# Kernel tuning notes

Measured on AMD Instinct MI355X. Metric: run time of the kernel, lower is better.

## Reference

```python
import jax, jax.numpy as jnp
import numpy as np

B, S, D = 2, 2048, 1024
H = 16
HD = D // H  # 64


def setup_inputs() -> dict:
    key = jax.random.key(0)
    k1, k2, k3, k4, k5, k6 = jax.random.split(key, 6)
    hidden_states = jax.random.normal(k1, (B, S, D), dtype=jnp.float32)
    attention_mask = jax.random.randint(k2, (B, S), 0, 2, dtype=jnp.int32)
    scale = 1.0 / np.sqrt(D)
    Wq = jax.random.normal(k3, (D, D), dtype=jnp.float32) * scale
    bq = jax.random.normal(k4, (D,), dtype=jnp.float32) * 0.02
    Wk = jax.random.normal(k5, (D, D), dtype=jnp.float32) * scale
    bk = jax.random.normal(k6, (D,), dtype=jnp.float32) * 0.02
    return {"hidden_states": hidden_states, "attention_mask": attention_mask,
            "Wq": Wq, "bq": bq, "Wk": Wk, "bk": bk}


def _split_heads(x):
    # [B, S, D] -> [B, H, S, HD]
    b, s, _ = x.shape
    return x.reshape(b, s, H, HD).transpose(0, 2, 1, 3)


def reference(hidden_states, attention_mask, Wq, bq, Wk, bk):
    dh = jnp.sqrt(jnp.float32(HD))
    q = _split_heads(hidden_states @ Wq + bq)            # [B,H,S,HD]
    k = _split_heads(hidden_states @ Wk + bk)            # [B,H,S,HD]
    v = q + k                                            # value = Q + K
    k_t = -jax.nn.log_sigmoid(-k)                        # negate the logsigmoid(-K) transform
    scores = jnp.einsum('bhqd,bhkd->bhqk', q, k_t) / dh  # [B,H,S,S]
    # mask applied on the QUERY axis (dim 2), broadcast over key axis (faithful to source)
    mask = (attention_mask[:, None, :, None] == 0)       # [B,1,S,1]
    scores = jnp.where(mask, jnp.float32(-10000.0), scores)
    probs = jax.nn.softmax(scores, axis=-1)              # dropout: eval mode (identity)
    ctx = jnp.einsum('bhqk,bhkd->bhqd', probs, v)        # [B,H,S,HD]
    ctx = ctx.transpose(0, 2, 1, 3).reshape(B, S, D)
    return ctx
```

## Files before the change

### kernel.cpp

```cpp
#include <hip/hip_runtime.h>
#include <hip/hip_bf16.h>

#define B_ 2
#define S_ 2048
#define D_ 1024
#define H_ 16
#define HD_ 64

typedef __attribute__((ext_vector_type(8))) short short8;
typedef __attribute__((ext_vector_type(4))) short short4v;
typedef __attribute__((ext_vector_type(4))) float float4v;

typedef const __attribute__((address_space(1))) void* gas_ptr;
typedef __attribute__((address_space(3))) void* las_ptr;

static __device__ inline void gl_lds16(const void* g, void* l) {
  __builtin_amdgcn_global_load_lds((gas_ptr)g, (las_ptr)l, 16, 0, 0);
}

static __device__ inline float b2f(__hip_bfloat16 h) { return __bfloat162float(h); }

static __device__ inline short f2bs(float x) {
  __hip_bfloat16 h = __float2bfloat16(x);
  union { __hip_bfloat16 h; short s; } u; u.h = h; return u.s;
}
static __device__ inline float bs2f(short s) {
  union { short s; __hip_bfloat16 h; } u; u.s = s; return __bfloat162float(u.h);
}
static __device__ inline short4v pk4(float a, float b, float c, float d) {
  union { __hip_bfloat162 h[2]; short4v s; } u;
  u.h[0] = __float22bfloat162_rn(float2{a, b});
  u.h[1] = __float22bfloat162_rn(float2{c, d});
  return u.s;
}

static __device__ inline float4v mfma32(short8 a, short8 b, float4v c) {
  return __builtin_amdgcn_mfma_f32_16x16x32_bf16(a, b, c, 0, 0, 0);
}
static __device__ inline float4v mfma16(short4v a, short4v b, float4v c) {
  return __builtin_amdgcn_mfma_f32_16x16x16bf16_1k(a, b, c, 0, 0, 0);
}

__global__ __launch_bounds__(256) void pre(
    const float* __restrict__ Wq, const float* __restrict__ Wk,
    __hip_bfloat16* __restrict__ Wqt, __hip_bfloat16* __restrict__ Wkt) {
  const float* W = blockIdx.z ? Wk : Wq;
  __hip_bfloat16* Wt = blockIdx.z ? Wkt : Wqt;
  __shared__ float t[64][65];
  const int n0 = blockIdx.x * 64, k0 = blockIdx.y * 64;
  const int c = threadIdx.x & 63, r0 = threadIdx.x >> 6;
  for (int i = 0; i < 16; ++i) {
    const int r = i * 4 + r0;
    t[c][r] = W[(size_t)(k0 + r) * D_ + n0 + c];
  }
  __syncthreads();
  for (int i = 0; i < 16; ++i) {
    const int rr = i * 4 + r0;
    Wt[(size_t)(n0 + rr) * D_ + k0 + c] = __float2bfloat16(t[rr][c]);
  }
}

__global__ __launch_bounds__(512, 2) void gemm_fused(
    const float* __restrict__ hs,
    const __hip_bfloat16* __restrict__ Wqt, const __hip_bfloat16* __restrict__ Wkt,
    const float* __restrict__ bq, const float* __restrict__ bk,
    __hip_bfloat16* __restrict__ q_out, __hip_bfloat16* __restrict__ kt_out,
    __hip_bfloat16* __restrict__ vT) {
  const int id = blockIdx.x;
  const int mt = (id & 7) * 4 + ((id >> 3) & 3);
  const int nt = id >> 5;
  const int n0 = nt * 128, m0 = mt * 128;
  __shared__ __hip_bfloat16 As[2][128 * 32];
  __shared__ __hip_bfloat16 Bq[2][128 * 32];
  __shared__ __hip_bfloat16 Bk[2][128 * 32];
  const int tid = threadIdx.x, wid = tid >> 6, lane = tid & 63;
  const int wm = (wid >> 1) * 32, wn = (wid & 1) * 64;
  const int l15 = lane & 15, l4 = lane >> 4;
  const float4v zz = {0.f, 0.f, 0.f, 0.f};
  float4v accq[2][4], acck[2][4];
  for (int i = 0; i < 2; ++i)
    for (int j = 0; j < 4; ++j) { accq[i][j] = zz; acck[i][j] = zz; }
  const int lrow = wid * 16 + (lane >> 2);
  const int lk8 = (lane & 3) * 8;
  {
    const float* pa = hs + (size_t)(m0 + lrow) * D_ + lk8;
    const float4v a0 = ((const float4v*)pa)[0], a1 = ((const float4v*)pa)[1];
    short8 s;
    for (int j = 0; j < 4; ++j) { s[j] = f2bs(a0[j]); s[4 + j] = f2bs(a1[j]); }
    *(short8*)(As[0] + wid * 512 + lane * 8) = s;
    gl_lds16(Wqt + (size_t)(n0 + lrow) * D_ + lk8, Bq[0] + wid * 512);
    gl_lds16(Wkt + (size_t)(n0 + lrow) * D_ + lk8, Bk[0] + wid * 512);
  }
  int p = 0;
  for (int kb = 0; kb < 32; ++kb) {
    __syncthreads();
    if (kb < 31) {
      const int kc = (kb + 1) * 32 + lk8;
      gl_lds16(Wqt + (size_t)(n0 + lrow) * D_ + kc, Bq[p ^ 1] + wid * 512);
      gl_lds16(Wkt + (size_t)(n0 + lrow) * D_ + kc, Bk[p ^ 1] + wid * 512);
      const float* pa = hs + (size_t)(m0 + lrow) * D_ + kc;
      const float4v a0 = ((const float4v*)pa)[0], a1 = ((const float4v*)pa)[1];
      short8 s;
      for (int j = 0; j < 4; ++j) { s[j] = f2bs(a0[j]); s[4 + j] = f2bs(a1[j]); }
      *(short8*)(As[p ^ 1] + wid * 512 + lane * 8) = s;
    }
    short8 af[2], bfq[4], bfk[4];
    const int fo = l4 * 8;
    for (int rt = 0; rt < 2; ++rt)
      af[rt] = *(const short8*)(As[p] + (wm + rt * 16 + l15) * 32 + fo);
    for (int ct = 0; ct < 4; ++ct) {
      bfq[ct] = *(const short8*)(Bq[p] + (wn + ct * 16 + l15) * 32 + fo);
      bfk[ct] = *(const short8*)(Bk[p] + (wn + ct * 16 + l15) * 32 + fo);
    }
    for (int rt = 0; rt < 2; ++rt)
      for (int ct = 0; ct < 4; ++ct) {
        accq[rt][ct] = mfma32(af[rt], bfq[ct], accq[rt][ct]);
        acck[rt][ct] = mfma32(af[rt], bfk[ct], acck[rt][ct]);
      }
    p ^= 1;
  }
  float bvq[4], bvk[4];
  for (int ct = 0; ct < 4; ++ct) {
    bvq[ct] = bq[n0 + wn + ct * 16 + l15];
    bvk[ct] = bk[n0 + wn + ct * 16 + l15];
  }
  for (int rt = 0; rt < 2; ++rt)
    for (int ct = 0; ct < 4; ++ct) {
      const int col = n0 + wn + ct * 16 + l15;
      const int h = col >> 6, d = col & 63;
      const int rowb = m0 + wm + rt * 16 + l4 * 4;
      short4v vv;
      for (int r = 0; r < 4; ++r) {
        const int row = rowb + r;
        const float qv = accq[rt][ct][r] + bvq[ct];
        const float kv = acck[rt][ct][r] + bvk[ct];
        const float sp = fmaxf(kv, 0.f) + __logf(1.f + __expf(-fabsf(kv)));
        q_out[(size_t)row * D_ + col] = __float2bfloat16(qv);
        kt_out[(size_t)row * D_ + col] = __float2bfloat16(sp);
        vv[r] = f2bs(qv + kv);
      }
      const int b = rowb >> 11, s = rowb & 2047;
      const int sw = (s & ~63) | (((s >> 4) & 3) << 2) | (((s >> 2) & 3) << 4);
      *(short4v*)(vT + ((size_t)(b * H_ + h) * HD_ + d) * S_ + sw) = vv;
    }
}

__global__ __launch_bounds__(256, 2) void attn(
    const __hip_bfloat16* __restrict__ qb, const __hip_bfloat16* __restrict__ ktb,
    const __hip_bfloat16* __restrict__ vT, const int* __restrict__ mask,
    float* __restrict__ out) {
  __shared__ short smem[32768];
  const int id = blockIdx.x;
  const int xcd = id & 7;
  const int rest = id >> 3;
  const int q0 = (rest & 15) * 128;
  const int hb = (rest >> 4) * 8 + xcd;
  const int h = hb >> 1, b = hb & 1;
  const int tid = threadIdx.x, wid = tid >> 6, lane = tid & 63;
  const int l15 = lane & 15, l4 = lane >> 4;
  const __hip_bfloat16* qh = qb + (size_t)b * S_ * D_ + h * HD_;
  const __hip_bfloat16* kh = ktb + (size_t)b * S_ * D_ + h * HD_;
  const __hip_bfloat16* vh = vT + (size_t)(b * H_ + h) * HD_ * S_;
  const int srow = tid >> 2;
  const int b0 = tid & 3;
  const int sh = srow & 7;
  const int w0 = srow * 64 + ((b0 ^ sh) * 8);
  const int w1 = srow * 64 + (((b0 + 4) ^ sh) * 8);

  const int qlA = wid * 32 + l15, qlB = qlA + 16;
  const int qrA = q0 + qlA, qrB = q0 + qlB;
  const float SC = 0.125f * 1.44269504f;
  const float mqA = (mask[b * S_ + qrA] != 0) ? SC : 0.f;
  const float mqB = (mask[b * S_ + qrB] != 0) ? SC : 0.f;
  const short8 rA0 = *(const short8*)(qh + (size_t)qrA * D_ + l4 * 8);
  const short8 rA1 = *(const short8*)(qh + (size_t)qrA * D_ + 32 + l4 * 8);
  const short8 rB0 = *(const short8*)(qh + (size_t)qrB * D_ + l4 * 8);
  const short8 rB1 = *(const short8*)(qh + (size_t)qrB * D_ + 32 + l4 * 8);
  short8 bqA0, bqA1, bqB0, bqB1;
  for (int j = 0; j < 8; ++j) {
    bqA0[j] = f2bs(bs2f(rA0[j]) * mqA);
    bqA1[j] = f2bs(bs2f(rA1[j]) * mqA);
    bqB0[j] = f2bs(bs2f(rB0[j]) * mqB);
    bqB1[j] = f2bs(bs2f(rB1[j]) * mqB);
  }

  const int lsh = l15 & 7;
  const int ak0off = l15 * 64 + ((l4 ^ lsh) * 8);
  const int ak1off = l15 * 64 + (((l4 + 4) ^ lsh) * 8);
  const int vb0off = ((2 * l4) ^ lsh) * 8;
  const int vb1off = ((2 * l4 + 1) ^ lsh) * 8;

  const float4v zz = {0.f, 0.f, 0.f, 0.f};
  float4v oaccA[4] = {zz, zz, zz, zz};
  float4v oaccB[4] = {zz, zz, zz, zz};
  float lsumA = 0.f, lsumB = 0.f;

  short8 gk0[2], gk1[2], gv0[2], gv1[2];
#pragma unroll
  for (int u = 0; u < 2; ++u) {
    gk0[u] = *(const short8*)(kh + (size_t)(u * 64 + srow) * D_ + b0 * 8);
    gk1[u] = *(const short8*)(kh + (size_t)(u * 64 + srow) * D_ + b0 * 8 + 32);
    gv0[u] = *(const short8*)(vh + (size_t)srow * S_ + u * 64 + b0 * 8);
    gv1[u] = *(const short8*)(vh + (size_t)srow * S_ + u * 64 + b0 * 8 + 32);
  }

  int p = 0;
  for (int c = 0; c < 16; ++c) {
    short* bufp = smem + p * 16384;
#pragma unroll
    for (int u = 0; u < 2; ++u) {
      *(short8*)(bufp + u * 4096 + w0) = gk0[u];
      *(short8*)(bufp + u * 4096 + w1) = gk1[u];
      *(short8*)(bufp + 8192 + u * 4096 + w0) = gv0[u];
      *(short8*)(bufp + 8192 + u * 4096 + w1) = gv1[u];
    }
    __syncthreads();
    if (c < 15) {
      const int kb = (c + 1) * 128;
#pragma unroll
      for (int u = 0; u < 2; ++u) {
        gk0[u] = *(const short8*)(kh + (size_t)(kb + u * 64 + srow) * D_ + b0 * 8);
        gk1[u] = *(const short8*)(kh + (size_t)(kb + u * 64 + srow) * D_ + b0 * 8 + 32);
        gv0[u] = *(const short8*)(vh + (size_t)srow * S_ + kb + u * 64 + b0 * 8);
        gv1[u] = *(const short8*)(vh + (size_t)srow * S_ + kb + u * 64 + b0 * 8 + 32);
      }
    }
#pragma unroll
    for (int u = 0; u < 2; ++u) {
      const short* kbase = bufp + u * 4096;
      const short* vbase = bufp + 8192 + u * 4096;
      short4v pA[4], pB[4];
#pragma unroll
      for (int t = 0; t < 4; ++t) {
        const short8 ak0 = *(const short8*)(kbase + t * 1024 + ak0off);
        const short8 ak1 = *(const short8*)(kbase + t * 1024 + ak1off);
        float4v cA = zz, cB = zz;
        cA = mfma32(ak0, bqA0, cA);
        cA = mfma32(ak1, bqA1, cA);
        cB = mfma32(ak0, bqB0, cB);
        cB = mfma32(ak1, bqB1, cB);
        float eA[4], eB[4];
#pragma unroll
        for (int r = 0; r < 4; ++r) {
          eA[r] = __builtin_amdgcn_exp2f(cA[r]); lsumA += eA[r];
          eB[r] = __builtin_amdgcn_exp2f(cB[r]); lsumB += eB[r];
        }
        pA[t] = pk4(eA[0], eA[1], eA[2], eA[3]);
        pB[t] = pk4(eB[0], eB[1], eB[2], eB[3]);
      }
#pragma unroll
      for (int dt = 0; dt < 4; ++dt) {
        const int rb = (dt * 16 + l15) * 64;
        const short8 av0 = *(const short8*)(vbase + rb + vb0off);
        const short8 av1 = *(const short8*)(vbase + rb + vb1off);
        const short4v a0 = {av0[0], av0[1], av0[2], av0[3]};
        const short4v a1 = {av0[4], av0[5], av0[6], av0[7]};
        const short4v a2 = {av1[0], av1[1], av1[2], av1[3]};
        const short4v a3 = {av1[4], av1[5], av1[6], av1[7]};
        oaccA[dt] = mfma16(a0, pA[0], oaccA[dt]);
        oaccB[dt] = mfma16(a0, pB[0], oaccB[dt]);
        oaccA[dt] = mfma16(a1, pA[1], oaccA[dt]);
        oaccB[dt] = mfma16(a1, pB[1], oaccB[dt]);
        oaccA[dt] = mfma16(a2, pA[2], oaccA[dt]);
        oaccB[dt] = mfma16(a2, pB[2], oaccB[dt]);
        oaccA[dt] = mfma16(a3, pA[3], oaccA[dt]);
        oaccB[dt] = mfma16(a3, pB[3], oaccB[dt]);
      }
    }
    p ^= 1;
  }
  float lA = lsumA + __shfl_xor(lsumA, 16); lA += __shfl_xor(lA, 32);
  float lB = lsumB + __shfl_xor(lsumB, 16); lB += __shfl_xor(lB, 32);
  __syncthreads();
  float* mbuf = (float*)smem;
  float* mlb = (float*)smem + 128 * 68;
#pragma unroll
  for (int dt = 0; dt < 4; ++dt)
#pragma unroll
    for (int r = 0; r < 4; ++r) {
      mbuf[qlA * 68 + dt * 16 + l4 * 4 + r] = oaccA[dt][r];
      mbuf[qlB * 68 + dt * 16 + l4 * 4 + r] = oaccB[dt][r];
    }
  if (l4 == 0) { mlb[qlA] = lA; mlb[qlB] = lB; }
  __syncthreads();
  const int qq = tid >> 1;
  const int dg = (tid & 1) * 32;
  const float li = 1.f / mlb[qq];
  float* orow = out + (size_t)(b * S_ + q0 + qq) * D_ + h * HD_ + dg;
#pragma unroll
  for (int i = 0; i < 8; ++i) {
    float4v v = *(const float4v*)&mbuf[qq * 68 + dg + i * 4];
#pragma unroll
    for (int r = 0; r < 4; ++r) v[r] *= li;
    *(float4v*)(orow + i * 4) = v;
  }
}

extern "C" void kernel_launch(void* const* d_in, const int* in_sizes, int n_in,
                              void* d_out, int out_size, void* d_ws, size_t ws_size,
                              hipStream_t stream) {
  const float* hs = (const float*)d_in[0];
  const int* mask = (const int*)d_in[1];
  const float* Wq = (const float*)d_in[2];
  const float* bq = (const float*)d_in[3];
  const float* Wk = (const float*)d_in[4];
  const float* bk = (const float*)d_in[5];
  float* out = (float*)d_out;
  char* ws = (char*)d_ws;
  const size_t MB = 1u << 20;
  __hip_bfloat16* q_b = (__hip_bfloat16*)(ws + 0 * MB);
  __hip_bfloat16* k_b = (__hip_bfloat16*)(ws + 8 * MB);
  __hip_bfloat16* vT  = (__hip_bfloat16*)(ws + 16 * MB);
  __hip_bfloat16* Wqt = (__hip_bfloat16*)(ws + 24 * MB);
  __hip_bfloat16* Wkt = (__hip_bfloat16*)(ws + 26 * MB);

  pre<<<dim3(16, 16, 2), 256, 0, stream>>>(Wq, Wk, Wqt, Wkt);
  gemm_fused<<<dim3(256), 512, 0, stream>>>(hs, Wqt, Wkt, bq, bk, q_b, k_b, vT);
  attn<<<dim3(512), 256, 0, stream>>>(q_b, k_b, vT, mask, out);
}
```

Before: 163.2 us.

## Software-pipeline attention inner loop across sub-tiles with MFMA priority hints

Restructures the per-chunk inner loop so that all K/V LDS fragments are loaded up front. The QK MFMAs of the second sub-tile are interleaved with the PV MFMAs of the first, while the exp2 softmax work runs between them. Wraps MFMA bursts in s_setprio to raise wave priority during matrix work. The aim is to overlap exp/VALU work and LDS latency with matrix-core work, at the cost of higher register pressure that may reduce occupancy or cause spills.

```diff
diff --git a/kernel.cpp b/kernel.cpp
--- a/kernel.cpp
+++ b/kernel.cpp
@@ -225,48 +225,116 @@
         gv1[u] = *(const short8*)(vh + (size_t)srow * S_ + kb + u * 64 + b0 * 8 + 32);
       }
     }
-#pragma unroll
-    for (int u = 0; u < 2; ++u) {
-      const short* kbase = bufp + u * 4096;
-      const short* vbase = bufp + 8192 + u * 4096;
-      short4v pA[4], pB[4];
-#pragma unroll
-      for (int t = 0; t < 4; ++t) {
-        const short8 ak0 = *(const short8*)(kbase + t * 1024 + ak0off);
-        const short8 ak1 = *(const short8*)(kbase + t * 1024 + ak1off);
-        float4v cA = zz, cB = zz;
-        cA = mfma32(ak0, bqA0, cA);
-        cA = mfma32(ak1, bqA1, cA);
-        cB = mfma32(ak0, bqB0, cB);
-        cB = mfma32(ak1, bqB1, cB);
-        float eA[4], eB[4];
-#pragma unroll
-        for (int r = 0; r < 4; ++r) {
-          eA[r] = __builtin_amdgcn_exp2f(cA[r]); lsumA += eA[r];
-          eB[r] = __builtin_amdgcn_exp2f(cB[r]); lsumB += eB[r];
-        }
-        pA[t] = pk4(eA[0], eA[1], eA[2], eA[3]);
-        pB[t] = pk4(eB[0], eB[1], eB[2], eB[3]);
-      }
-#pragma unroll
-      for (int dt = 0; dt < 4; ++dt) {
-        const int rb = (dt * 16 + l15) * 64;
-        const short8 av0 = *(const short8*)(vbase + rb + vb0off);
-        const short8 av1 = *(const short8*)(vbase + rb + vb1off);
-        const short4v a0 = {av0[0], av0[1], av0[2], av0[3]};
-        const short4v a1 = {av0[4], av0[5], av0[6], av0[7]};
-        const short4v a2 = {av1[0], av1[1], av1[2], av1[3]};
-        const short4v a3 = {av1[4], av1[5], av1[6], av1[7]};
-        oaccA[dt] = mfma16(a0, pA[0], oaccA[dt]);
-        oaccB[dt] = mfma16(a0, pB[0], oaccB[dt]);
-        oaccA[dt] = mfma16(a1, pA[1], oaccA[dt]);
-        oaccB[dt] = mfma16(a1, pB[1], oaccB[dt]);
-        oaccA[dt] = mfma16(a2, pA[2], oaccA[dt]);
-        oaccB[dt] = mfma16(a2, pB[2], oaccB[dt]);
-        oaccA[dt] = mfma16(a3, pA[3], oaccA[dt]);
-        oaccB[dt] = mfma16(a3, pB[3], oaccB[dt]);
-      }
-    }
+    const short* k0b = bufp;
+    const short* k1b = bufp + 4096;
+    const short* v0b = bufp + 8192;
+    const short* v1b = bufp + 12288;
+
+    short8 ak0_0[4], ak1_0[4], ak0_1[4], ak1_1[4];
+    short8 av0_0[4], av1_0[4], av0_1[4], av1_1[4];
+#pragma unroll
+    for (int t = 0; t < 4; ++t) {
+      ak0_0[t] = *(const short8*)(k0b + t * 1024 + ak0off);
+      ak1_0[t] = *(const short8*)(k0b + t * 1024 + ak1off);
+    }
+#pragma unroll
+    for (int dt = 0; dt < 4; ++dt) {
+      const int rb = (dt * 16 + l15) * 64;
+      av0_0[dt] = *(const short8*)(v0b + rb + vb0off);
+      av1_0[dt] = *(const short8*)(v0b + rb + vb1off);
+    }
+#pragma unroll
+    for (int t = 0; t < 4; ++t) {
+      ak0_1[t] = *(const short8*)(k1b + t * 1024 + ak0off);
+      ak1_1[t] = *(const short8*)(k1b + t * 1024 + ak1off);
+    }
+
+    float4v c0A[4], c0B[4];
+    __builtin_amdgcn_s_setprio(1);
+#pragma unroll
+    for (int t = 0; t < 4; ++t) {
+      float4v cA = zz, cB = zz;
+      cA = mfma32(ak0_0[t], bqA0, cA);
+      cA = mfma32(ak1_0[t], bqA1, cA);
+      cB = mfma32(ak0_0[t], bqB0, cB);
+      cB = mfma32(ak1_0[t], bqB1, cB);
+      c0A[t] = cA; c0B[t] = cB;
+    }
+    __builtin_amdgcn_s_setprio(0);
+    short4v pA0[4], pB0[4];
+#pragma unroll
+    for (int t = 0; t < 4; ++t) {
+      float eA[4], eB[4];
+#pragma unroll
+      for (int r = 0; r < 4; ++r) {
+        eA[r] = __builtin_amdgcn_exp2f(c0A[t][r]); lsumA += eA[r];
+        eB[r] = __builtin_amdgcn_exp2f(c0B[t][r]); lsumB += eB[r];
+      }
+      pA0[t] = pk4(eA[0], eA[1], eA[2], eA[3]);
+      pB0[t] = pk4(eB[0], eB[1], eB[2], eB[3]);
+    }
+#pragma unroll
+    for (int dt = 0; dt < 4; ++dt) {
+      const int rb = (dt * 16 + l15) * 64;
+      av0_1[dt] = *(const short8*)(v1b + rb + vb0off);
+      av1_1[dt] = *(const short8*)(v1b + rb + vb1off);
+    }
+    float4v c1A[4], c1B[4];
+    __builtin_amdgcn_s_setprio(1);
+#pragma unroll
+    for (int t = 0; t < 4; ++t) {
+      float4v cA = zz, cB = zz;
+      cA = mfma32(ak0_1[t], bqA0, cA);
+      cA = mfma32(ak1_1[t], bqA1, cA);
+      cB = mfma32(ak0_1[t], bqB0, cB);
+      cB = mfma32(ak1_1[t], bqB1, cB);
+      c1A[t] = cA; c1B[t] = cB;
+    }
+#pragma unroll
+    for (int dt = 0; dt < 4; ++dt) {
+      const short4v a0 = {av0_0[dt][0], av0_0[dt][1], av0_0[dt][2], av0_0[dt][3]};
+      const short4v a1 = {av0_0[dt][4], av0_0[dt][5], av0_0[dt][6], av0_0[dt][7]};
+      const short4v a2 = {av1_0[dt][0], av1_0[dt][1], av1_0[dt][2], av1_0[dt][3]};
+      const short4v a3 = {av1_0[dt][4], av1_0[dt][5], av1_0[dt][6], av1_0[dt][7]};
+      oaccA[dt] = mfma16(a0, pA0[0], oaccA[dt]);
+      oaccB[dt] = mfma16(a0, pB0[0], oaccB[dt]);
+      oaccA[dt] = mfma16(a1, pA0[1], oaccA[dt]);
+      oaccB[dt] = mfma16(a1, pB0[1], oaccB[dt]);
+      oaccA[dt] = mfma16(a2, pA0[2], oaccA[dt]);
+      oaccB[dt] = mfma16(a2, pB0[2], oaccB[dt]);
+      oaccA[dt] = mfma16(a3, pA0[3], oaccA[dt]);
+      oaccB[dt] = mfma16(a3, pB0[3], oaccB[dt]);
+    }
+    __builtin_amdgcn_s_setprio(0);
+    short4v pA1[4], pB1[4];
+#pragma unroll
+    for (int t = 0; t < 4; ++t) {
+      float eA[4], eB[4];
+#pragma unroll
+      for (int r = 0; r < 4; ++r) {
+        eA[r] = __builtin_amdgcn_exp2f(c1A[t][r]); lsumA += eA[r];
+        eB[r] = __builtin_amdgcn_exp2f(c1B[t][r]); lsumB += eB[r];
+      }
+      pA1[t] = pk4(eA[0], eA[1], eA[2], eA[3]);
+      pB1[t] = pk4(eB[0], eB[1], eB[2], eB[3]);
+    }
+    __builtin_amdgcn_s_setprio(1);
+#pragma unroll
+    for (int dt = 0; dt < 4; ++dt) {
+      const short4v a0 = {av0_1[dt][0], av0_1[dt][1], av0_1[dt][2], av0_1[dt][3]};
+      const short4v a1 = {av0_1[dt][4], av0_1[dt][5], av0_1[dt][6], av0_1[dt][7]};
+      const short4v a2 = {av1_1[dt][0], av1_1[dt][1], av1_1[dt][2], av1_1[dt][3]};
+      const short4v a3 = {av1_1[dt][4], av1_1[dt][5], av1_1[dt][6], av1_1[dt][7]};
+      oaccA[dt] = mfma16(a0, pA1[0], oaccA[dt]);
+      oaccB[dt] = mfma16(a0, pB1[0], oaccB[dt]);
+      oaccA[dt] = mfma16(a1, pA1[1], oaccA[dt]);
+      oaccB[dt] = mfma16(a1, pB1[1], oaccB[dt]);
+      oaccA[dt] = mfma16(a2, pA1[2], oaccA[dt]);
+      oaccB[dt] = mfma16(a2, pB1[2], oaccB[dt]);
+      oaccA[dt] = mfma16(a3, pA1[3], oaccA[dt]);
+      oaccB[dt] = mfma16(a3, pB1[3], oaccB[dt]);
+    }
+    __builtin_amdgcn_s_setprio(0);
     p ^= 1;
   }
   float lA = lsumA + __shfl_xor(lsumA, 16); lA += __shfl_xor(lA, 32);
```

New measurement: 167.3 us. 1.03x slower.

## Pre-convert hidden states to bf16 and stream A tile via async LDS loads with swizzle

Applied to the files above, without the earlier changes.

Adds a separate conversion kernel that turns hidden_states into bf16 once, so the GEMM can load its A tile through direct global-to-LDS loads like the weights instead of loading fp32 through registers and converting. It also adds an XOR swizzle on the GEMM's LDS k-chunks and changes the swizzle pattern in the attention kernel's K/V staging, both aimed at reducing LDS bank conflicts. The cost is an extra kernel launch plus a full fp32 read and bf16 write of hidden_states.

```diff
diff --git a/kernel.cpp b/kernel.cpp
--- a/kernel.cpp
+++ b/kernel.cpp
@@ -39,6 +39,17 @@
 }
 static __device__ inline float4v mfma16(short4v a, short4v b, float4v c) {
   return __builtin_amdgcn_mfma_f32_16x16x16bf16_1k(a, b, c, 0, 0, 0);
+}
+
+__global__ __launch_bounds__(256) void cvt(
+    const float* __restrict__ in, __hip_bfloat16* __restrict__ out) {
+  const size_t i = ((size_t)blockIdx.x * 256 + threadIdx.x) * 8;
+  const float4v a0 = ((const float4v*)(in + i))[0];
+  const float4v a1 = ((const float4v*)(in + i))[1];
+  short8 s;
+#pragma unroll
+  for (int j = 0; j < 4; ++j) { s[j] = f2bs(a0[j]); s[4 + j] = f2bs(a1[j]); }
+  *(short8*)(out + i) = s;
 }
 
 __global__ __launch_bounds__(256) void pre(
@@ -61,7 +72,7 @@
 }
 
 __global__ __launch_bounds__(512, 2) void gemm_fused(
-    const float* __restrict__ hs,
+    const __hip_bfloat16* __restrict__ hsb,
     const __hip_bfloat16* __restrict__ Wqt, const __hip_bfloat16* __restrict__ Wkt,
     const float* __restrict__ bq, const float* __restrict__ bk,
     __hip_bfloat16* __restrict__ q_out, __hip_bfloat16* __restrict__ kt_out,
@@ -81,13 +92,9 @@
   for (int i = 0; i < 2; ++i)
     for (int j = 0; j < 4; ++j) { accq[i][j] = zz; acck[i][j] = zz; }
   const int lrow = wid * 16 + (lane >> 2);
-  const int lk8 = (lane & 3) * 8;
+  const int lk8 = (((lane & 3) ^ ((lane >> 3) & 3)) * 8);
   {
-    const float* pa = hs + (size_t)(m0 + lrow) * D_ + lk8;
-    const float4v a0 = ((const float4v*)pa)[0], a1 = ((const float4v*)pa)[1];
-    short8 s;
-    for (int j = 0; j < 4; ++j) { s[j] = f2bs(a0[j]); s[4 + j] = f2bs(a1[j]); }
-    *(short8*)(As[0] + wid * 512 + lane * 8) = s;
+    gl_lds16(hsb + (size_t)(m0 + lrow) * D_ + lk8, As[0] + wid * 512);
     gl_lds16(Wqt + (size_t)(n0 + lrow) * D_ + lk8, Bq[0] + wid * 512);
     gl_lds16(Wkt + (size_t)(n0 + lrow) * D_ + lk8, Bk[0] + wid * 512);
   }
@@ -96,16 +103,12 @@
     __syncthreads();
     if (kb < 31) {
       const int kc = (kb + 1) * 32 + lk8;
+      gl_lds16(hsb + (size_t)(m0 + lrow) * D_ + kc, As[p ^ 1] + wid * 512);
       gl_lds16(Wqt + (size_t)(n0 + lrow) * D_ + kc, Bq[p ^ 1] + wid * 512);
       gl_lds16(Wkt + (size_t)(n0 + lrow) * D_ + kc, Bk[p ^ 1] + wid * 512);
-      const float* pa = hs + (size_t)(m0 + lrow) * D_ + kc;
-      const float4v a0 = ((const float4v*)pa)[0], a1 = ((const float4v*)pa)[1];
-      short8 s;
-      for (int j = 0; j < 4; ++j) { s[j] = f2bs(a0[j]); s[4 + j] = f2bs(a1[j]); }
-      *(short8*)(As[p ^ 1] + wid * 512 + lane * 8) = s;
     }
     short8 af[2], bfq[4], bfk[4];
-    const int fo = l4 * 8;
+    const int fo = ((l4 ^ ((l15 >> 1) & 3)) * 8);
     for (int rt = 0; rt < 2; ++rt)
       af[rt] = *(const short8*)(As[p] + (wm + rt * 16 + l15) * 32 + fo);
     for (int ct = 0; ct < 4; ++ct) {
@@ -163,9 +166,9 @@
   const __hip_bfloat16* vh = vT + (size_t)(b * H_ + h) * HD_ * S_;
   const int srow = tid >> 2;
   const int b0 = tid & 3;
-  const int sh = srow & 7;
-  const int w0 = srow * 64 + ((b0 ^ sh) * 8);
-  const int w1 = srow * 64 + (((b0 + 4) ^ sh) * 8);
+  const int ssw = ((srow & 1) << 2) | ((srow >> 1) & 3);
+  const int w0 = srow * 64 + ((b0 ^ ssw) * 8);
+  const int w1 = srow * 64 + (((b0 + 4) ^ ssw) * 8);
 
   const int qlA = wid * 32 + l15, qlB = qlA + 16;
   const int qrA = q0 + qlA, qrB = q0 + qlB;
@@ -184,11 +187,11 @@
     bqB1[j] = f2bs(bs2f(rB1[j]) * mqB);
   }
 
-  const int lsh = l15 & 7;
-  const int ak0off = l15 * 64 + ((l4 ^ lsh) * 8);
-  const int ak1off = l15 * 64 + (((l4 + 4) ^ lsh) * 8);
-  const int vb0off = ((2 * l4) ^ lsh) * 8;
-  const int vb1off = ((2 * l4 + 1) ^ lsh) * 8;
+  const int lsw = ((l15 & 1) << 2) | ((l15 >> 1) & 3);
+  const int ak0off = l15 * 64 + ((l4 ^ lsw) * 8);
+  const int ak1off = l15 * 64 + (((l4 + 4) ^ lsw) * 8);
+  const int vb0off = ((2 * l4) ^ lsw) * 8;
+  const int vb1off = ((2 * l4 + 1) ^ lsw) * 8;
 
   const float4v zz = {0.f, 0.f, 0.f, 0.f};
   float4v oaccA[4] = {zz, zz, zz, zz};
@@ -313,8 +316,10 @@
   __hip_bfloat16* vT  = (__hip_bfloat16*)(ws + 16 * MB);
   __hip_bfloat16* Wqt = (__hip_bfloat16*)(ws + 24 * MB);
   __hip_bfloat16* Wkt = (__hip_bfloat16*)(ws + 26 * MB);
-
+  __hip_bfloat16* hsb = (__hip_bfloat16*)(ws + 28 * MB);
+
+  cvt<<<dim3(2048), 256, 0, stream>>>(hs, hsb);
   pre<<<dim3(16, 16, 2), 256, 0, stream>>>(Wq, Wk, Wqt, Wkt);
-  gemm_fused<<<dim3(256), 512, 0, stream>>>(hs, Wqt, Wkt, bq, bk, q_b, k_b, vT);
+  gemm_fused<<<dim3(256), 512, 0, stream>>>(hsb, Wqt, Wkt, bq, bk, q_b, k_b, vT);
   attn<<<dim3(512), 256, 0, stream>>>(q_b, k_b, vT, mask, out);
 }
```

Measured after the change: 161.4 us. Within noise of the previous version (-1.1%).
